# Optimization experiments

Measured on AMD Instinct MI355X. Metric: run time of the kernel, lower is better.

Reference implementation:

```python
import jax, jax.numpy as jnp
import numpy as np

NUM_USERS = 60000
NUM_ITEMS = 40000
NUM_NODES = NUM_USERS + NUM_ITEMS
EMB = 64
HID = 32
N_EDGES = 1600000
BATCH = 16384


def setup_inputs() -> dict:
    key = jax.random.key(0)
    ks = jax.random.split(key, 16)
    def xavier(k, shape):
        fan_in, fan_out = shape[1], shape[0]
        lim = float(np.sqrt(6.0 / (fan_in + fan_out)))
        return jax.random.uniform(k, shape, jnp.float32, -lim, lim)
    return {
        "user_ids": jax.random.randint(ks[0], (BATCH,), 0, NUM_USERS),
        "item_ids": jax.random.randint(ks[1], (BATCH,), 0, NUM_ITEMS),
        "adj_rows": jax.random.randint(ks[2], (N_EDGES,), 0, NUM_NODES),
        "adj_cols": jax.random.randint(ks[3], (N_EDGES,), 0, NUM_NODES),
        "adj_vals": jax.random.uniform(ks[4], (N_EDGES,), jnp.float32),
        # embeddings (xavier_uniform, matching init_weights)
        "user_emb_w": xavier(ks[5], (NUM_USERS, EMB)),
        "item_emb_w": xavier(ks[6], (NUM_ITEMS, EMB)),
        # GC layer 1: 64 -> 32 ; GC layer 2: 32 -> 64
        "gc1_w": xavier(ks[7], (HID, EMB)),
        "gc1_b": jnp.zeros((HID,), jnp.float32),
        "gc2_w": xavier(ks[8], (EMB, HID)),
        "gc2_b": jnp.zeros((EMB,), jnp.float32),
        # predictor: Linear(2*EMB -> HID), ReLU, Linear(HID -> 1), Sigmoid
        "p1_w": xavier(ks[9], (HID, 2 * EMB)),
        "p1_b": jnp.zeros((HID,), jnp.float32),
        "p2_w": xavier(ks[10], (1, HID)),
        "p2_b": jnp.zeros((1,), jnp.float32),
    }


def _gc_layer(x, rows, cols, vals, w, b):
    # dense linear then spmm: out[i] = sum_e vals[e] * h[cols[e]] grouped by rows[e]
    h = x @ w.T + b                                # [N, out_dim]
    msg = vals[:, None] * h[cols]                  # [E, out_dim] gather (memory-bound)
    agg = jax.ops.segment_sum(msg, rows, num_segments=NUM_NODES)
    return jax.nn.relu(agg)                        # dropout in eval mode = identity


def reference(user_ids, item_ids, adj_rows, adj_cols, adj_vals,
              user_emb_w, item_emb_w, gc1_w, gc1_b, gc2_w, gc2_b,
              p1_w, p1_b, p2_w, p2_b):
    node_feat = jnp.concatenate([user_emb_w, item_emb_w], axis=0)  # [N, EMB]
    h = _gc_layer(node_feat, adj_rows, adj_cols, adj_vals, gc1_w, gc1_b)
    h = _gc_layer(h, adj_rows, adj_cols, adj_vals, gc2_w, gc2_b)
    final_user_emb = h[:NUM_USERS]
    final_item_emb = h[NUM_USERS:]
    bu = final_user_emb[user_ids]                  # [B, EMB]
    bi = final_item_emb[item_ids]                  # [B, EMB]
    z = jnp.concatenate([bu, bi], axis=1)          # [B, 2*EMB]
    z = jax.nn.relu(z @ p1_w.T + p1_b)             # [B, HID]
    scores = jax.nn.sigmoid(z @ p2_w.T + p2_b).squeeze(-1)  # [B]
    return (scores, final_user_emb, final_item_emb)
```

## Files before the change

### kernel.cpp

```cpp
#include <hip/hip_runtime.h>
#include <hip/hip_bf16.h>

#define NUM_USERS 60000
#define NUM_ITEMS 40000
#define NUM_NODES 100000
#define EMB 64
#define HID 32
#define N_EDGES 1600000
#define BATCH 16384

#define TILE 128
#define NBUCK 782
#define CAPB 3072
#define BLOCK_E 4096
#define NBLK_A 391
#define EPT 8
#define EPT_B (CAPB / 256)

#define WS_CUR    0
#define WS_BEND   800
#define WS_ROFF   1600
#define WS_BINNED 101952
#define WS_H1B    4906560
#define WS_A1B    6506560
#define WS_G      8106560
#define WS_SUMV   11306560

static __device__ __forceinline__ unsigned short f2bf(float f) {
    union { float f; unsigned u; } x; x.f = f;
    unsigned u = x.u;
    return (unsigned short)((u + 0x7FFFu + ((u >> 16) & 1u)) >> 16);
}
static __device__ __forceinline__ unsigned pack2bf(float lo, float hi) {
    return (unsigned)f2bf(lo) | ((unsigned)f2bf(hi) << 16);
}
static __device__ __forceinline__ float bflo(unsigned u) {
    union { unsigned v; float f; } x; x.v = u << 16; return x.f;
}
static __device__ __forceinline__ float bfhi(unsigned u) {
    union { unsigned v; float f; } x; x.v = u & 0xFFFF0000u; return x.f;
}

__global__ __launch_bounds__(1024) void k_initcur(unsigned* __restrict__ cur)
{
    int t = threadIdx.x;
    if (t < NBUCK) cur[t] = (unsigned)t * CAPB;
}

__global__ __launch_bounds__(512) void k_partA(
    const int* __restrict__ rows, const int* __restrict__ cols,
    const float* __restrict__ vals,
    unsigned* __restrict__ cursor, uint2* __restrict__ binned)
{
    __shared__ unsigned cnt[NBUCK];
    __shared__ unsigned offs[NBUCK];
    __shared__ unsigned gbase[NBUCK];
    __shared__ unsigned scanbuf[1024];
    __shared__ uint2    staged[BLOCK_E];
    __shared__ unsigned dstarr[BLOCK_E];

    int t = threadIdx.x;
    for (int i = t; i < NBUCK; i += 512) cnt[i] = 0u;
    __syncthreads();

    unsigned eb = blockIdx.x * BLOCK_E;
    unsigned bb[EPT], rk[EPT];
    uint2    pr[EPT];
    #pragma unroll
    for (int i = 0; i < EPT; i++) {
        unsigned e = eb + (unsigned)(i * 512 + t);
        if (e < N_EDGES) {
            unsigned r = (unsigned)rows[e];
            bb[i] = r >> 7;
            pr[i] = make_uint2(((r & 127u) << 17) | (unsigned)cols[e],
                               __float_as_uint(vals[e]));
            rk[i] = atomicAdd(&cnt[bb[i]], 1u);
        } else {
            bb[i] = 0xFFFFFFFFu;
        }
    }
    __syncthreads();

    unsigned c0 = (t < NBUCK) ? cnt[t] : 0u;
    unsigned c1 = (t + 512 < NBUCK) ? cnt[t + 512] : 0u;
    scanbuf[t] = c0; scanbuf[t + 512] = c1;
    __syncthreads();
    #pragma unroll
    for (int ofs = 1; ofs < 1024; ofs <<= 1) {
        unsigned a0 = (t >= ofs) ? scanbuf[t - ofs] : 0u;
        unsigned a1 = (t + 512 >= ofs) ? scanbuf[t + 512 - ofs] : 0u;
        __syncthreads();
        scanbuf[t] += a0; scanbuf[t + 512] += a1;
        __syncthreads();
    }
    if (t < NBUCK) offs[t] = scanbuf[t] - c0;
    if (t + 512 < NBUCK) offs[t + 512] = scanbuf[t + 512] - c1;
    __syncthreads();

    for (int b = t; b < NBUCK; b += 512) {
        unsigned c = cnt[b];
        gbase[b] = c ? atomicAdd(&cursor[b], c) : 0u;
    }
    __syncthreads();

    #pragma unroll
    for (int i = 0; i < EPT; i++) {
        if (bb[i] != 0xFFFFFFFFu) {
            unsigned s = offs[bb[i]] + rk[i];
            staged[s] = pr[i];
            dstarr[s] = gbase[bb[i]] + rk[i];
        }
    }
    __syncthreads();

    unsigned total = (eb + BLOCK_E <= N_EDGES) ? (unsigned)BLOCK_E
                                               : (N_EDGES - eb);
    for (unsigned s = t; s < total; s += 512)
        binned[dstarr[s]] = staged[s];
}

__global__ __launch_bounds__(256) void k_partB(
    const unsigned* __restrict__ cursor,
    uint2* __restrict__ binned,
    unsigned* __restrict__ roff, unsigned* __restrict__ bend)
{
    __shared__ uint2    ob[CAPB];
    __shared__ unsigned cnt[TILE];
    __shared__ unsigned sc[TILE];
    __shared__ unsigned offs[TILE];
    __shared__ unsigned totpad;

    int t = threadIdx.x;
    int nb = blockIdx.x;
    unsigned gs = (unsigned)nb * CAPB;
    unsigned count = cursor[nb] - gs;
    if (count > CAPB - TILE) count = CAPB - TILE;

    for (int i = t; i < TILE; i += 256) cnt[i] = 0u;
    __syncthreads();

    unsigned rl_[EPT_B], rk_[EPT_B];
    uint2    pp_[EPT_B];
    #pragma unroll
    for (int it = 0; it < EPT_B; it++) {
        unsigned s = (unsigned)t + it * 256u;
        if (s < count) {
            uint2 p = binned[gs + s];
            unsigned rl = p.x >> 17;
            pp_[it] = p;
            rl_[it] = rl;
            rk_[it] = atomicAdd(&cnt[rl], 1u);
        } else {
            rl_[it] = 0xFFFFFFFFu;
        }
    }
    __syncthreads();

    unsigned c  = (t < TILE) ? cnt[t] : 0u;
    unsigned pc = (c + 1u) & ~1u;
    if (t < TILE) sc[t] = pc;
    __syncthreads();
    #pragma unroll
    for (int ofs = 1; ofs < TILE; ofs <<= 1) {
        unsigned a = 0u;
        if (t < TILE && t >= ofs) a = sc[t - ofs];
        __syncthreads();
        if (t < TILE) sc[t] += a;
        __syncthreads();
    }
    if (t < TILE) offs[t] = sc[t] - pc;
    if (t == TILE - 1) totpad = sc[t];
    __syncthreads();

    for (int i = t; i < TILE; i += 256) {
        int n = nb * TILE + i;
        if (n <= NUM_NODES) roff[n] = gs + offs[i];
    }
    if (t == 0) bend[nb] = gs + totpad;

    if (t < TILE && (c & 1u)) ob[offs[t] + c] = make_uint2(0u, 0u);

    #pragma unroll
    for (int it = 0; it < EPT_B; it++) {
        if (rl_[it] != 0xFFFFFFFFu)
            ob[offs[rl_[it]] + rk_[it]] = pp_[it];
    }
    __syncthreads();
    unsigned tp = totpad;
    for (unsigned s = (unsigned)t; s < tp; s += 256)
        binned[gs + s] = ob[s];
}

template<bool LAYER1>
__global__ __launch_bounds__(256) void k_agg32(
    const unsigned* __restrict__ roff, const unsigned* __restrict__ bend,
    const uint2* __restrict__ binned,
    const unsigned* __restrict__ H,
    unsigned* __restrict__ outb,
    float* __restrict__ outf,
    float* __restrict__ sumv_out)
{
    int wave = threadIdx.x >> 6;
    int lane = threadIdx.x & 63;
    int n = blockIdx.x * 4 + wave;
    int g = lane >> 3;
    int q = lane & 7;
    unsigned s = roff[n];
    unsigned e = ((n & 127) == 127) ? bend[n >> 7] : roff[n + 1];
    float4 acc = make_float4(0.f, 0.f, 0.f, 0.f);
    float sv = 0.f;
    for (unsigned k = s + 2u * (unsigned)g; k < e; k += 16u) {
        uint4 pp = *reinterpret_cast<const uint4*>(&binned[k]);
        float va = __uint_as_float(pp.y);
        float vb = __uint_as_float(pp.w);
        uint2 ha = *(reinterpret_cast<const uint2*>(H + (size_t)(pp.x & 0x1FFFFu) * 16) + q);
        uint2 hb = *(reinterpret_cast<const uint2*>(H + (size_t)(pp.z & 0x1FFFFu) * 16) + q);
        acc.x = fmaf(va, bflo(ha.x), acc.x);
        acc.y = fmaf(va, bfhi(ha.x), acc.y);
        acc.z = fmaf(va, bflo(ha.y), acc.z);
        acc.w = fmaf(va, bfhi(ha.y), acc.w);
        acc.x = fmaf(vb, bflo(hb.x), acc.x);
        acc.y = fmaf(vb, bfhi(hb.x), acc.y);
        acc.z = fmaf(vb, bflo(hb.y), acc.z);
        acc.w = fmaf(vb, bfhi(hb.y), acc.w);
        if (!LAYER1) sv += va + vb;
    }
    #pragma unroll
    for (int m = 8; m < 64; m <<= 1) {
        acc.x += __shfl_xor(acc.x, m);
        acc.y += __shfl_xor(acc.y, m);
        acc.z += __shfl_xor(acc.z, m);
        acc.w += __shfl_xor(acc.w, m);
        if (!LAYER1) sv += __shfl_xor(sv, m);
    }
    if (g == 0) {
        if (LAYER1) {
            acc.x = fmaxf(acc.x, 0.f); acc.y = fmaxf(acc.y, 0.f);
            acc.z = fmaxf(acc.z, 0.f); acc.w = fmaxf(acc.w, 0.f);
            uint2 o = make_uint2(pack2bf(acc.x, acc.y), pack2bf(acc.z, acc.w));
            *(reinterpret_cast<uint2*>(outb + (size_t)n * 16) + q) = o;
        } else {
            reinterpret_cast<float4*>(outf + (size_t)n * HID)[q] = acc;
            if (q == 0) sumv_out[n] = sv;
        }
    }
}

__global__ __launch_bounds__(256) void k_linear1(
    const float* __restrict__ ue, const float* __restrict__ ie,
    const float* __restrict__ w, const float* __restrict__ b,
    unsigned* __restrict__ out)
{
    __shared__ float ws[HID * EMB];
    __shared__ float bs[HID];
    for (int i = threadIdx.x; i < HID * EMB; i += 256) ws[i] = w[i];
    if (threadIdx.x < HID) bs[threadIdx.x] = b[threadIdx.x];
    __syncthreads();

    int n = blockIdx.x * 256 + threadIdx.x;
    if (n >= NUM_NODES) return;
    const float* row = (n < NUM_USERS) ? ue + (size_t)n * EMB
                                       : ie + (size_t)(n - NUM_USERS) * EMB;
    float x[EMB];
    #pragma unroll
    for (int k4 = 0; k4 < EMB / 4; k4++) {
        float4 v = reinterpret_cast<const float4*>(row)[k4];
        x[4*k4+0] = v.x; x[4*k4+1] = v.y; x[4*k4+2] = v.z; x[4*k4+3] = v.w;
    }
    const float4* ws4 = reinterpret_cast<const float4*>(ws);
    float acc[HID];
    #pragma unroll
    for (int j = 0; j < HID; j++) {
        float a = bs[j];
        #pragma unroll
        for (int k4 = 0; k4 < EMB / 4; k4++) {
            float4 wv = ws4[j * (EMB/4) + k4];
            a = fmaf(wv.x, x[4*k4+0], a);
            a = fmaf(wv.y, x[4*k4+1], a);
            a = fmaf(wv.z, x[4*k4+2], a);
            a = fmaf(wv.w, x[4*k4+3], a);
        }
        acc[j] = a;
    }
    uint4* o4 = reinterpret_cast<uint4*>(out + (size_t)n * 16);
    #pragma unroll
    for (int j8 = 0; j8 < 4; j8++) {
        uint4 o;
        o.x = pack2bf(acc[8*j8+0], acc[8*j8+1]);
        o.y = pack2bf(acc[8*j8+2], acc[8*j8+3]);
        o.z = pack2bf(acc[8*j8+4], acc[8*j8+5]);
        o.w = pack2bf(acc[8*j8+6], acc[8*j8+7]);
        o4[j8] = o;
    }
}

__global__ __launch_bounds__(256) void k_linear2_post(
    const float* __restrict__ G, const float* __restrict__ sumv,
    const float* __restrict__ w, const float* __restrict__ b,
    float* __restrict__ out)
{
    __shared__ float ws[EMB * HID];
    __shared__ float bs[EMB];
    for (int i = threadIdx.x; i < EMB * HID; i += 256) ws[i] = w[i];
    if (threadIdx.x < EMB) bs[threadIdx.x] = b[threadIdx.x];
    __syncthreads();

    int n = blockIdx.x * 256 + threadIdx.x;
    if (n >= NUM_NODES) return;
    const float* row = G + (size_t)n * HID;
    float sv = sumv[n];
    float x[HID];
    #pragma unroll
    for (int k4 = 0; k4 < HID / 4; k4++) {
        float4 v = reinterpret_cast<const float4*>(row)[k4];
        x[4*k4+0] = v.x; x[4*k4+1] = v.y; x[4*k4+2] = v.z; x[4*k4+3] = v.w;
    }
    const float4* ws4 = reinterpret_cast<const float4*>(ws);
    float acc[EMB];
    #pragma unroll
    for (int j = 0; j < EMB; j++) {
        float a = sv * bs[j];
        #pragma unroll
        for (int k4 = 0; k4 < HID / 4; k4++) {
            float4 wv = ws4[j * (HID/4) + k4];
            a = fmaf(wv.x, x[4*k4+0], a);
            a = fmaf(wv.y, x[4*k4+1], a);
            a = fmaf(wv.z, x[4*k4+2], a);
            a = fmaf(wv.w, x[4*k4+3], a);
        }
        acc[j] = fmaxf(a, 0.f);
    }
    float4* o4 = reinterpret_cast<float4*>(out + (size_t)n * EMB);
    #pragma unroll
    for (int j4 = 0; j4 < EMB / 4; j4++)
        o4[j4] = make_float4(acc[4*j4], acc[4*j4+1], acc[4*j4+2], acc[4*j4+3]);
}

__global__ __launch_bounds__(256) void k_mlp(
    const int* __restrict__ uids, const int* __restrict__ iids,
    const float* __restrict__ uemb, const float* __restrict__ iemb,
    const float* __restrict__ p1w, const float* __restrict__ p1b,
    const float* __restrict__ p2w, const float* __restrict__ p2b,
    float* __restrict__ scores)
{
    __shared__ float w1t[2 * EMB * HID];
    __shared__ float zt[8][2 * EMB];
    __shared__ float b1s[HID];
    __shared__ float w2s[HID];

    for (int i = threadIdx.x; i < HID * 2 * EMB; i += 256) {
        int j = i >> 7;
        int k = i & 127;
        int k4 = k >> 2, c = k & 3;
        w1t[k4 * 128 + j * 4 + c] = p1w[i];
    }
    if (threadIdx.x < HID) {
        b1s[threadIdx.x] = p1b[threadIdx.x];
        w2s[threadIdx.x] = p2w[threadIdx.x];
    }
    __syncthreads();

    int lg = threadIdx.x >> 5;
    int j  = threadIdx.x & 31;
    int s  = blockIdx.x * 8 + lg;

    {
        int u  = uids[s];
        int it = iids[s];
        const float* bu = uemb + (size_t)u * EMB;
        const float* bi = iemb + (size_t)it * EMB;
        float* zs = zt[lg];
        zs[j]      = bu[j];
        zs[32 + j] = bu[32 + j];
        zs[64 + j] = bi[j];
        zs[96 + j] = bi[32 + j];
    }
    __syncthreads();

    const float*  zs = zt[lg];
    const float4* w4 = reinterpret_cast<const float4*>(w1t);
    const float4* z4 = reinterpret_cast<const float4*>(zs);
    float a = b1s[j];
    #pragma unroll
    for (int k4 = 0; k4 < 32; k4++) {
        float4 wv = w4[k4 * 32 + j];
        float4 zv = z4[k4];
        a = fmaf(wv.x, zv.x, a);
        a = fmaf(wv.y, zv.y, a);
        a = fmaf(wv.z, zv.z, a);
        a = fmaf(wv.w, zv.w, a);
    }
    a = fmaxf(a, 0.f);
    float part = a * w2s[j];
    #pragma unroll
    for (int m = 16; m >= 1; m >>= 1) part += __shfl_xor(part, m);
    if (j == 0) scores[s] = 1.f / (1.f + expf(-(part + p2b[0])));
}

extern "C" void kernel_launch(void* const* d_in, const int* in_sizes, int n_in,
                              void* d_out, int out_size, void* d_ws, size_t ws_size,
                              hipStream_t stream)
{
    const int*   user_ids = (const int*)  d_in[0];
    const int*   item_ids = (const int*)  d_in[1];
    const int*   adj_rows = (const int*)  d_in[2];
    const int*   adj_cols = (const int*)  d_in[3];
    const float* adj_vals = (const float*)d_in[4];
    const float* user_emb = (const float*)d_in[5];
    const float* item_emb = (const float*)d_in[6];
    const float* gc1_w    = (const float*)d_in[7];
    const float* gc1_b    = (const float*)d_in[8];
    const float* gc2_w    = (const float*)d_in[9];
    const float* gc2_b    = (const float*)d_in[10];
    const float* p1_w     = (const float*)d_in[11];
    const float* p1_b     = (const float*)d_in[12];
    const float* p2_w     = (const float*)d_in[13];
    const float* p2_b     = (const float*)d_in[14];

    float* out     = (float*)d_out;
    float* scores  = out;
    float* emb_out = out + BATCH;

    unsigned* ws_u   = (unsigned*)d_ws;
    unsigned* cur    = ws_u + WS_CUR;
    unsigned* bend   = ws_u + WS_BEND;
    unsigned* roff   = ws_u + WS_ROFF;
    uint2*    binned = (uint2*)(ws_u + WS_BINNED);
    unsigned* H1B    = ws_u + WS_H1B;
    unsigned* A1B    = ws_u + WS_A1B;
    float*    G      = (float*)(ws_u + WS_G);
    float*    SUMV   = (float*)(ws_u + WS_SUMV);

    k_initcur<<<1, 1024, 0, stream>>>(cur);
    k_partA<<<NBLK_A, 512, 0, stream>>>(adj_rows, adj_cols, adj_vals,
                                        cur, binned);
    k_partB<<<NBUCK, 256, 0, stream>>>(cur, binned, roff, bend);

    k_linear1<<<(NUM_NODES + 255) / 256, 256, 0, stream>>>(
        user_emb, item_emb, gc1_w, gc1_b, H1B);
    k_agg32<true><<<NUM_NODES / 4, 256, 0, stream>>>(
        roff, bend, binned, H1B, A1B, nullptr, nullptr);

    k_agg32<false><<<NUM_NODES / 4, 256, 0, stream>>>(
        roff, bend, binned, A1B, nullptr, G, SUMV);
    k_linear2_post<<<(NUM_NODES + 255) / 256, 256, 0, stream>>>(
        G, SUMV, gc2_w, gc2_b, emb_out);

    k_mlp<<<BATCH / 8, 256, 0, stream>>>(
        user_ids, item_ids, emb_out, emb_out + (size_t)NUM_USERS * EMB,
        p1_w, p1_b, p2_w, p2_b, scores);
}
```

Measured before the change: 258.5 us.

## Fuse layer-1 linear into partition kernel and layer-2 linear into aggregation

Moves the first dense projection (64->32, bf16 output) into the tail of the CSR partition kernel, so each bucket block also projects its 128 nodes. The second dense projection plus ReLU moves into the layer-2 aggregation kernel, using per-wave shared buffers and a padded weight tile. This removes two kernel launches and the G/SUMV intermediate round trip through global memory. In exchange, the partition kernel uses more shared memory and registers, and the aggregation kernel gains a block-wide barrier and a per-block load of the weight matrix.

```diff
diff --git a/kernel.cpp b/kernel.cpp
--- a/kernel.cpp
+++ b/kernel.cpp
@@ -23,8 +23,6 @@
 #define WS_BINNED 101952
 #define WS_H1B    4906560
 #define WS_A1B    6506560
-#define WS_G      8106560
-#define WS_SUMV   11306560
 
 static __device__ __forceinline__ unsigned short f2bf(float f) {
     union { float f; unsigned u; } x; x.f = f;
@@ -122,13 +120,18 @@
 __global__ __launch_bounds__(256) void k_partB(
     const unsigned* __restrict__ cursor,
     uint2* __restrict__ binned,
-    unsigned* __restrict__ roff, unsigned* __restrict__ bend)
+    unsigned* __restrict__ roff, unsigned* __restrict__ bend,
+    const float* __restrict__ ue, const float* __restrict__ ie,
+    const float* __restrict__ w1, const float* __restrict__ b1,
+    unsigned* __restrict__ h1b)
 {
     __shared__ uint2    ob[CAPB];
     __shared__ unsigned cnt[TILE];
     __shared__ unsigned sc[TILE];
     __shared__ unsigned offs[TILE];
     __shared__ unsigned totpad;
+    __shared__ float    ws1[HID * EMB];
+    __shared__ float    bs1[HID];
 
     int t = threadIdx.x;
     int nb = blockIdx.x;
@@ -136,6 +139,8 @@
     unsigned count = cursor[nb] - gs;
     if (count > CAPB - TILE) count = CAPB - TILE;
 
+    for (int i = t; i < HID * EMB; i += 256) ws1[i] = w1[i];
+    if (t < HID) bs1[t] = b1[t];
     for (int i = t; i < TILE; i += 256) cnt[i] = 0u;
     __syncthreads();
 
@@ -189,6 +194,49 @@
     unsigned tp = totpad;
     for (unsigned s = (unsigned)t; s < tp; s += 256)
         binned[gs + s] = ob[s];
+
+    {
+        int i = t & 127, h = t >> 7;
+        int n = nb * TILE + i;
+        if (n < NUM_NODES) {
+            const float* row = (n < NUM_USERS)
+                ? ue + (size_t)n * EMB
+                : ie + (size_t)(n - NUM_USERS) * EMB;
+            float x[EMB];
+            #pragma unroll
+            for (int k4 = 0; k4 < EMB / 4; k4++) {
+                float4 v = reinterpret_cast<const float4*>(row)[k4];
+                x[4*k4+0] = v.x; x[4*k4+1] = v.y;
+                x[4*k4+2] = v.z; x[4*k4+3] = v.w;
+            }
+            const float4* ws4 = reinterpret_cast<const float4*>(ws1);
+            float acc[16];
+            #pragma unroll
+            for (int jj = 0; jj < 16; jj++) {
+                int j = h * 16 + jj;
+                float a = bs1[j];
+                #pragma unroll
+                for (int k4 = 0; k4 < EMB / 4; k4++) {
+                    float4 wv = ws4[j * (EMB/4) + k4];
+                    a = fmaf(wv.x, x[4*k4+0], a);
+                    a = fmaf(wv.y, x[4*k4+1], a);
+                    a = fmaf(wv.z, x[4*k4+2], a);
+                    a = fmaf(wv.w, x[4*k4+3], a);
+                }
+                acc[jj] = a;
+            }
+            uint4* o4 = reinterpret_cast<uint4*>(h1b + (size_t)n * 16 + h * 8);
+            #pragma unroll
+            for (int q8 = 0; q8 < 2; q8++) {
+                uint4 o;
+                o.x = pack2bf(acc[8*q8+0], acc[8*q8+1]);
+                o.y = pack2bf(acc[8*q8+2], acc[8*q8+3]);
+                o.z = pack2bf(acc[8*q8+4], acc[8*q8+5]);
+                o.w = pack2bf(acc[8*q8+6], acc[8*q8+7]);
+                o4[q8] = o;
+            }
+        }
+    }
 }
 
 template<bool LAYER1>
@@ -197,11 +245,24 @@
     const uint2* __restrict__ binned,
     const unsigned* __restrict__ H,
     unsigned* __restrict__ outb,
-    float* __restrict__ outf,
-    float* __restrict__ sumv_out)
-{
-    int wave = threadIdx.x >> 6;
-    int lane = threadIdx.x & 63;
+    const float* __restrict__ w2, const float* __restrict__ b2,
+    float* __restrict__ oute)
+{
+    __shared__ float w2s[EMB * 33];
+    __shared__ float bs2[EMB];
+    __shared__ float gbuf[4][32];
+
+    int t = threadIdx.x;
+    if (!LAYER1) {
+        for (int idx = t; idx < EMB * HID; idx += 256) {
+            int j = idx >> 5, k = idx & 31;
+            w2s[j * 33 + k] = w2[idx];
+        }
+        if (t < EMB) bs2[t] = b2[t];
+    }
+
+    int wave = t >> 6;
+    int lane = t & 63;
     int n = blockIdx.x * 4 + wave;
     int g = lane >> 3;
     int q = lane & 7;
@@ -233,107 +294,29 @@
         acc.w += __shfl_xor(acc.w, m);
         if (!LAYER1) sv += __shfl_xor(sv, m);
     }
-    if (g == 0) {
-        if (LAYER1) {
+    if (LAYER1) {
+        if (g == 0) {
             acc.x = fmaxf(acc.x, 0.f); acc.y = fmaxf(acc.y, 0.f);
             acc.z = fmaxf(acc.z, 0.f); acc.w = fmaxf(acc.w, 0.f);
             uint2 o = make_uint2(pack2bf(acc.x, acc.y), pack2bf(acc.z, acc.w));
             *(reinterpret_cast<uint2*>(outb + (size_t)n * 16) + q) = o;
-        } else {
-            reinterpret_cast<float4*>(outf + (size_t)n * HID)[q] = acc;
-            if (q == 0) sumv_out[n] = sv;
-        }
-    }
-}
-
-__global__ __launch_bounds__(256) void k_linear1(
-    const float* __restrict__ ue, const float* __restrict__ ie,
-    const float* __restrict__ w, const float* __restrict__ b,
-    unsigned* __restrict__ out)
-{
-    __shared__ float ws[HID * EMB];
-    __shared__ float bs[HID];
-    for (int i = threadIdx.x; i < HID * EMB; i += 256) ws[i] = w[i];
-    if (threadIdx.x < HID) bs[threadIdx.x] = b[threadIdx.x];
-    __syncthreads();
-
-    int n = blockIdx.x * 256 + threadIdx.x;
-    if (n >= NUM_NODES) return;
-    const float* row = (n < NUM_USERS) ? ue + (size_t)n * EMB
-                                       : ie + (size_t)(n - NUM_USERS) * EMB;
-    float x[EMB];
-    #pragma unroll
-    for (int k4 = 0; k4 < EMB / 4; k4++) {
-        float4 v = reinterpret_cast<const float4*>(row)[k4];
-        x[4*k4+0] = v.x; x[4*k4+1] = v.y; x[4*k4+2] = v.z; x[4*k4+3] = v.w;
-    }
-    const float4* ws4 = reinterpret_cast<const float4*>(ws);
-    float acc[HID];
-    #pragma unroll
-    for (int j = 0; j < HID; j++) {
-        float a = bs[j];
+        }
+    } else {
+        if (g == 0) {
+            gbuf[wave][q * 4 + 0] = acc.x;
+            gbuf[wave][q * 4 + 1] = acc.y;
+            gbuf[wave][q * 4 + 2] = acc.z;
+            gbuf[wave][q * 4 + 3] = acc.w;
+        }
+        __syncthreads();
+        float a = sv * bs2[lane];
+        const float* wr = &w2s[lane * 33];
+        const float* gb = gbuf[wave];
         #pragma unroll
-        for (int k4 = 0; k4 < EMB / 4; k4++) {
-            float4 wv = ws4[j * (EMB/4) + k4];
-            a = fmaf(wv.x, x[4*k4+0], a);
-            a = fmaf(wv.y, x[4*k4+1], a);
-            a = fmaf(wv.z, x[4*k4+2], a);
-            a = fmaf(wv.w, x[4*k4+3], a);
-        }
-        acc[j] = a;
-    }
-    uint4* o4 = reinterpret_cast<uint4*>(out + (size_t)n * 16);
-    #pragma unroll
-    for (int j8 = 0; j8 < 4; j8++) {
-        uint4 o;
-        o.x = pack2bf(acc[8*j8+0], acc[8*j8+1]);
-        o.y = pack2bf(acc[8*j8+2], acc[8*j8+3]);
-        o.z = pack2bf(acc[8*j8+4], acc[8*j8+5]);
-        o.w = pack2bf(acc[8*j8+6], acc[8*j8+7]);
-        o4[j8] = o;
-    }
-}
-
-__global__ __launch_bounds__(256) void k_linear2_post(
-    const float* __restrict__ G, const float* __restrict__ sumv,
-    const float* __restrict__ w, const float* __restrict__ b,
-    float* __restrict__ out)
-{
-    __shared__ float ws[EMB * HID];
-    __shared__ float bs[EMB];
-    for (int i = threadIdx.x; i < EMB * HID; i += 256) ws[i] = w[i];
-    if (threadIdx.x < EMB) bs[threadIdx.x] = b[threadIdx.x];
-    __syncthreads();
-
-    int n = blockIdx.x * 256 + threadIdx.x;
-    if (n >= NUM_NODES) return;
-    const float* row = G + (size_t)n * HID;
-    float sv = sumv[n];
-    float x[HID];
-    #pragma unroll
-    for (int k4 = 0; k4 < HID / 4; k4++) {
-        float4 v = reinterpret_cast<const float4*>(row)[k4];
-        x[4*k4+0] = v.x; x[4*k4+1] = v.y; x[4*k4+2] = v.z; x[4*k4+3] = v.w;
-    }
-    const float4* ws4 = reinterpret_cast<const float4*>(ws);
-    float acc[EMB];
-    #pragma unroll
-    for (int j = 0; j < EMB; j++) {
-        float a = sv * bs[j];
-        #pragma unroll
-        for (int k4 = 0; k4 < HID / 4; k4++) {
-            float4 wv = ws4[j * (HID/4) + k4];
-            a = fmaf(wv.x, x[4*k4+0], a);
-            a = fmaf(wv.y, x[4*k4+1], a);
-            a = fmaf(wv.z, x[4*k4+2], a);
-            a = fmaf(wv.w, x[4*k4+3], a);
-        }
-        acc[j] = fmaxf(a, 0.f);
-    }
-    float4* o4 = reinterpret_cast<float4*>(out + (size_t)n * EMB);
-    #pragma unroll
-    for (int j4 = 0; j4 < EMB / 4; j4++)
-        o4[j4] = make_float4(acc[4*j4], acc[4*j4+1], acc[4*j4+2], acc[4*j4+3]);
+        for (int k = 0; k < HID; k++)
+            a = fmaf(gb[k], wr[k], a);
+        oute[(size_t)n * EMB + lane] = fmaxf(a, 0.f);
+    }
 }
 
 __global__ __launch_bounds__(256) void k_mlp(
@@ -428,23 +411,18 @@
     uint2*    binned = (uint2*)(ws_u + WS_BINNED);
     unsigned* H1B    = ws_u + WS_H1B;
     unsigned* A1B    = ws_u + WS_A1B;
-    float*    G      = (float*)(ws_u + WS_G);
-    float*    SUMV   = (float*)(ws_u + WS_SUMV);
 
     k_initcur<<<1, 1024, 0, stream>>>(cur);
     k_partA<<<NBLK_A, 512, 0, stream>>>(adj_rows, adj_cols, adj_vals,
                                         cur, binned);
-    k_partB<<<NBUCK, 256, 0, stream>>>(cur, binned, roff, bend);
-
-    k_linear1<<<(NUM_NODES + 255) / 256, 256, 0, stream>>>(
-        user_emb, item_emb, gc1_w, gc1_b, H1B);
+    k_partB<<<NBUCK, 256, 0, stream>>>(cur, binned, roff, bend,
+                                       user_emb, item_emb, gc1_w, gc1_b, H1B);
+
     k_agg32<true><<<NUM_NODES / 4, 256, 0, stream>>>(
-        roff, bend, binned, H1B, A1B, nullptr, nullptr);
+        roff, bend, binned, H1B, A1B, nullptr, nullptr, nullptr);
 
     k_agg32<false><<<NUM_NODES / 4, 256, 0, stream>>>(
-        roff, bend, binned, A1B, nullptr, G, SUMV);
-    k_linear2_post<<<(NUM_NODES + 255) / 256, 256, 0, stream>>>(
-        G, SUMV, gc2_w, gc2_b, emb_out);
+        roff, bend, binned, A1B, nullptr, gc2_w, gc2_b, emb_out);
 
     k_mlp<<<BATCH / 8, 256, 0, stream>>>(
         user_ids, item_ids, emb_out, emb_out + (size_t)NUM_USERS * EMB,
```

After: 259.3 us. No clear change (+0.3%).
